# Kernel tuning notes

Measured on AMD Instinct MI355X. Metric: run time of the kernel, lower is better.

The kernel has to match this reference:

```python
import jax, jax.numpy as jnp
import numpy as np

NUM_HEADS = 16
ROPE_THETA = 10000.0


def apply_rope(x):
    # x: (B, H, T, hd), interleaved-pair RoPE (rotary-embedding-torch convention)
    T, hd = x.shape[-2], x.shape[-1]
    inv_freq = 1.0 / (ROPE_THETA ** (jnp.arange(0, hd, 2, dtype=jnp.float32) / hd))  # (hd/2,)
    ang = jnp.arange(T, dtype=jnp.float32)[:, None] * inv_freq[None, :]  # (T, hd/2)
    cos, sin = jnp.cos(ang), jnp.sin(ang)
    x1 = x[..., 0::2]
    x2 = x[..., 1::2]
    r1 = x1 * cos - x2 * sin
    r2 = x1 * sin + x2 * cos
    return jnp.stack([r1, r2], axis=-1).reshape(x.shape)


def setup_inputs() -> dict:
    key = jax.random.key(0)
    ks = jax.random.split(key, 8)
    L, S, B, E = 2048, 2048, 2, 1024
    sc = 1.0 / np.sqrt(E)
    return {
        "query": jax.random.normal(ks[0], (L, B, E), jnp.float32),
        "key": jax.random.normal(ks[1], (S, B, E), jnp.float32),
        "value": jax.random.normal(ks[2], (S, B, E), jnp.float32),
        "key_padding_mask": jnp.zeros((B, S), dtype=bool),
        "Wq": jax.random.normal(ks[3], (E, E), jnp.float32) * sc,
        "bq": jnp.zeros((E,), jnp.float32),
        "Wk": jax.random.normal(ks[4], (E, E), jnp.float32) * sc,
        "bk": jnp.zeros((E,), jnp.float32),
        "Wv": jax.random.normal(ks[5], (E, E), jnp.float32) * sc,
        "bv": jnp.zeros((E,), jnp.float32),
        "Wo": jax.random.normal(ks[6], (E, E), jnp.float32) * sc,
        "bo": jnp.zeros((E,), jnp.float32),
    }


def reference(query, key, value, key_padding_mask, Wq, bq, Wk, bk, Wv, bv, Wo, bo):
    L, B, E = query.shape
    S = key.shape[0]
    H = NUM_HEADS
    hd = E // H
    # projections (torch Linear: x @ W.T + b)
    Q = query @ Wq.T + bq  # (L, B, E)
    K = key @ Wk.T + bk    # (S, B, E)
    V = value @ Wv.T + bv  # (S, B, E)
    # (T, B, E) -> (B, H, T, hd)
    Q = Q.reshape(L, B, H, hd).transpose(1, 2, 0, 3)
    K = K.reshape(S, B, H, hd).transpose(1, 2, 0, 3)
    V = V.reshape(S, B, H, hd).transpose(1, 2, 0, 3)
    Q = apply_rope(Q)
    K = apply_rope(K)
    scores = jnp.einsum("bhld,bhsd->bhls", Q, K) / jnp.sqrt(jnp.float32(hd))
    scores = jnp.where(key_padding_mask[:, None, None, :], -jnp.inf, scores)
    attn = jax.nn.softmax(scores, axis=-1)
    out = jnp.einsum("bhls,bhsd->bhld", attn, V)  # (B, H, L, hd)
    out = out.transpose(2, 0, 1, 3).reshape(L, B, E)
    return out @ Wo.T + bo
```

## Files before the change

kernel.cpp:

```cpp
#include <hip/hip_runtime.h>
#include <hip/hip_bf16.h>

typedef __hip_bfloat16 bf16;
typedef short bf16x8 __attribute__((ext_vector_type(8)));
typedef float f32x4 __attribute__((ext_vector_type(4)));
typedef short s4 __attribute__((ext_vector_type(4)));

#define LL 2048
#define SS 2048
#define EE 1024
#define HH 16
#define HD 64
#define MM (LL * 2)

static __device__ __forceinline__ short f2bs(float f) {
  bf16 h = __float2bfloat16(f);
  short u;
  __builtin_memcpy(&u, &h, 2);
  return u;
}

static __device__ __forceinline__ void st8(bf16* p, float4 x, float4 y) {
  bf16x8 v;
  v[0] = f2bs(x.x); v[1] = f2bs(x.y); v[2] = f2bs(x.z); v[3] = f2bs(x.w);
  v[4] = f2bs(y.x); v[5] = f2bs(y.y); v[6] = f2bs(y.z); v[7] = f2bs(y.w);
  *(bf16x8*)p = v;
}

#define GLL16(gp, lp) __builtin_amdgcn_global_load_lds(                        \
    (const __attribute__((address_space(1))) void*)(gp),                       \
    (__attribute__((address_space(3))) void*)(lp), 16, 0, 0)

__global__ __launch_bounds__(256) void prep_kernel(
    float2* __restrict__ tab, const unsigned char* __restrict__ m,
    float* __restrict__ mf,
    const float* __restrict__ s0, const float* __restrict__ s1,
    const float* __restrict__ s2, const float* __restrict__ s3,
    bf16* __restrict__ wdst) {
  const int bid = blockIdx.x;
  if (bid < 256) {
    int i = bid * 256 + threadIdx.x;
    int pos = i >> 5, fi = i & 31;
    float freq = expf(-(float)fi * (9.210340371976184f / 32.0f));
    float ang = (float)pos * freq;
    float s, c;
    sincosf(ang, &s, &c);
    tab[i] = make_float2(c, s);
  } else if (bid < 272) {
    int i = (bid - 256) * 256 + threadIdx.x;
    if (i < 2 * SS) mf[i] = m[i] ? -1e30f : 0.f;
  } else {
    int b2 = bid - 272;
    int sel = b2 >> 10;
    const float* src = (sel == 0) ? s0 : (sel == 1) ? s1 : (sel == 2) ? s2 : s3;
    size_t loc = ((size_t)(b2 & 1023) * 256 + threadIdx.x) * 4;
    float4 v = *(const float4*)(src + loc);
    s4 p;
    p[0] = f2bs(v.x); p[1] = f2bs(v.y); p[2] = f2bs(v.z); p[3] = f2bs(v.w);
    *(s4*)(wdst + (size_t)sel * EE * EE + loc) = p;
  }
}

template<int MODE, bool XB16, bool WB16>
__global__ __launch_bounds__(256) void proj_kernel(
    const void* __restrict__ Xv, const void* __restrict__ Wv,
    const float* __restrict__ bias, void* __restrict__ dstv,
    const float2* __restrict__ tab)
{
  const int w = threadIdx.x >> 6;
  const int lane = threadIdx.x & 63;
  const int l15 = lane & 15, quad = lane >> 4;
  const int tm = blockIdx.x * 128 + w * 32;
  const int tn = blockIdx.y * 64;

  const size_t aoff0 = (size_t)(tm + l15) * EE + quad * 8;
  const size_t aoff1 = aoff0 + (size_t)16 * EE;
  const size_t woff  = (size_t)(tn + l15) * EE + quad * 8;

  f32x4 zero4 = {0.f, 0.f, 0.f, 0.f};
  f32x4 acc[2][4];
#pragma unroll
  for (int mi = 0; mi < 2; ++mi)
#pragma unroll
    for (int ni = 0; ni < 4; ++ni) acc[mi][ni] = zero4;

  for (int k0 = 0; k0 < EE; k0 += 32) {
    bf16x8 a0, a1;
    if (XB16 || MODE == 3) {
      const bf16* Xb = (const bf16*)Xv;
      a0 = *(const bf16x8*)(Xb + aoff0 + k0);
      a1 = *(const bf16x8*)(Xb + aoff1 + k0);
    } else {
      const float* Xf = (const float*)Xv;
#pragma unroll
      for (int j = 0; j < 8; ++j) a0[j] = f2bs(Xf[aoff0 + k0 + j]);
#pragma unroll
      for (int j = 0; j < 8; ++j) a1[j] = f2bs(Xf[aoff1 + k0 + j]);
    }
#pragma unroll
    for (int ni = 0; ni < 4; ++ni) {
      bf16x8 bv;
      if (WB16) {
        const bf16* Wb = (const bf16*)Wv;
        bv = *(const bf16x8*)(Wb + woff + (size_t)ni * 16 * EE + k0);
      } else {
        const float* Wf = (const float*)Wv;
#pragma unroll
        for (int j = 0; j < 8; ++j) bv[j] = f2bs(Wf[woff + (size_t)ni * 16 * EE + k0 + j]);
      }
      acc[0][ni] = __builtin_amdgcn_mfma_f32_16x16x32_bf16(a0, bv, acc[0][ni], 0, 0, 0);
      acc[1][ni] = __builtin_amdgcn_mfma_f32_16x16x32_bf16(a1, bv, acc[1][ni], 0, 0, 0);
    }
  }

  float bz[4];
#pragma unroll
  for (int ni = 0; ni < 4; ++ni) bz[ni] = bias[tn + ni * 16 + l15];

#pragma unroll
  for (int mi = 0; mi < 2; ++mi) {
#pragma unroll
    for (int ni = 0; ni < 4; ++ni) {
      const int n = tn + ni * 16 + l15;
#pragma unroll
      for (int r = 0; r < 4; ++r) {
        const int m = tm + mi * 16 + quad * 4 + r;
        float v = acc[mi][ni][r] + bz[ni];
        if (MODE <= 1) {
          float other = __shfl_xor(v, 1, 64);
          int pos = m >> 1, b = m & 1, d = n & 63, h = n >> 6;
          float2 cs = tab[pos * 32 + (d >> 1)];
          float rv = (d & 1) ? (other * cs.y + v * cs.x) : (v * cs.x - other * cs.y);
          ((bf16*)dstv)[((size_t)(b * HH + h) * LL + pos) * HD + d] = __float2bfloat16(rv);
        } else if (MODE == 2) {
          int pos = m >> 1, b = m & 1, d = n & 63, h = n >> 6;
          ((bf16*)dstv)[((size_t)(b * HH + h) * HD + d) * SS + pos] = __float2bfloat16(v);
        } else {
          ((float*)dstv)[(size_t)m * EE + n] = v;
        }
      }
    }
  }
}

__global__ __launch_bounds__(256, 6) void qkv_kernel(
    const float* __restrict__ Xq, const float* __restrict__ Xk,
    const float* __restrict__ Xv, const bf16* __restrict__ Wb,
    const float* __restrict__ bq, const float* __restrict__ bk,
    const float* __restrict__ bv, bf16* __restrict__ Qr,
    bf16* __restrict__ Kr, bf16* __restrict__ Vt,
    const float2* __restrict__ tab)
{
  __shared__ __align__(16) bf16 As[2][4096];
  __shared__ __align__(16) bf16 Bs[2][2048];

  const int tid = threadIdx.x;
  const int w = tid >> 6;
  const int lane = tid & 63;
  const int l15 = lane & 15, quad = lane >> 4;
  const int id = blockIdx.x;
  const int z = id >> 9;
  const int g = id & 511;
  const int tmb = (g & 31) * 128;
  const int tn  = (g >> 5) * 64;

  const float* Xf = (z == 0) ? Xq : (z == 1) ? Xk : Xv;
  const bf16* Wm  = Wb + (size_t)z * EE * EE;
  const float* bias = (z == 0) ? bq : (z == 1) ? bk : bv;
  bf16* dst = (z == 0) ? Qr : (z == 1) ? Kr : Vt;

  const int ar = tid >> 2;
  const int akc = tid & 3;
  const float* gA0 = Xf + (size_t)(tmb + ar) * EE + akc * 8;
  const float* gA1 = gA0 + (size_t)64 * EE;
  const int aw0 = (ar >> 1) * 64 + (((((ar & 1) << 2) | akc) ^ ((ar >> 1) & 7)) * 8);
  const int aw1 = aw0 + 2048;

  const int ub = (lane & 7) ^ (lane >> 3);
  const bf16* gB = Wm + (size_t)(tn + w * 16 + 2 * (lane >> 3) + (ub >> 2)) * EE
                      + (ub & 3) * 8;

  const int arbase = (l15 >> 1) * 64 + (((((l15 & 1) << 2) | quad) ^ (l15 >> 1)) * 8);

  f32x4 zero4 = {0.f, 0.f, 0.f, 0.f};
  f32x4 acc[2][4];
#pragma unroll
  for (int mi = 0; mi < 2; ++mi)
#pragma unroll
    for (int ni = 0; ni < 4; ++ni) acc[mi][ni] = zero4;

  {
    float4 a00 = *(const float4*)(gA0);
    float4 a01 = *(const float4*)(gA0 + 4);
    float4 a10 = *(const float4*)(gA1);
    float4 a11 = *(const float4*)(gA1 + 4);
    GLL16(gB, (bf16*)&Bs[0][w * 512] + lane * 8);
    st8(&As[0][aw0], a00, a01);
    st8(&As[0][aw1], a10, a11);
  }
  __syncthreads();

  for (int t = 0; t < 32; ++t) {
    const int cur = t & 1;
    float4 a00, a01, a10, a11;
    if (t < 31) {
      const int k0 = (t + 1) * 32;
      a00 = *(const float4*)(gA0 + k0);
      a01 = *(const float4*)(gA0 + k0 + 4);
      a10 = *(const float4*)(gA1 + k0);
      a11 = *(const float4*)(gA1 + k0 + 4);
      GLL16(gB + k0, (bf16*)&Bs[cur ^ 1][w * 512] + lane * 8);
    }
    bf16x8 af0 = *(const bf16x8*)(&As[cur][w * 1024 + arbase]);
    bf16x8 af1 = *(const bf16x8*)(&As[cur][w * 1024 + 512 + arbase]);
#pragma unroll
    for (int ni = 0; ni < 4; ++ni) {
      bf16x8 bfr = *(const bf16x8*)(&Bs[cur][ni * 512 + arbase]);
      acc[0][ni] = __builtin_amdgcn_mfma_f32_16x16x32_bf16(af0, bfr, acc[0][ni], 0, 0, 0);
      acc[1][ni] = __builtin_amdgcn_mfma_f32_16x16x32_bf16(af1, bfr, acc[1][ni], 0, 0, 0);
    }
    if (t < 31) {
      st8(&As[cur ^ 1][aw0], a00, a01);
      st8(&As[cur ^ 1][aw1], a10, a11);
    }
    __syncthreads();
  }

  float bz[4];
#pragma unroll
  for (int ni = 0; ni < 4; ++ni) bz[ni] = bias[tn + ni * 16 + l15];

#pragma unroll
  for (int mi = 0; mi < 2; ++mi) {
#pragma unroll
    for (int ni = 0; ni < 4; ++ni) {
      const int n = tn + ni * 16 + l15;
#pragma unroll
      for (int r = 0; r < 4; ++r) {
        const int m = tmb + w * 32 + mi * 16 + quad * 4 + r;
        float v = acc[mi][ni][r] + bz[ni];
        if (z <= 1) {
          float other = __shfl_xor(v, 1, 64);
          int pos = m >> 1, b = m & 1, d = n & 63, h = n >> 6;
          float2 cs = tab[pos * 32 + (d >> 1)];
          float rv = (d & 1) ? (other * cs.y + v * cs.x) : (v * cs.x - other * cs.y);
          dst[((size_t)(b * HH + h) * LL + pos) * HD + d] = __float2bfloat16(rv);
        } else {
          int pos = m >> 1, b = m & 1, d = n & 63, h = n >> 6;
          dst[((size_t)(b * HH + h) * HD + d) * SS + pos] = __float2bfloat16(v);
        }
      }
    }
  }
}

__global__ __launch_bounds__(256, 4) void projo_kernel(
    const bf16* __restrict__ X, const bf16* __restrict__ W,
    const float* __restrict__ bias, float* __restrict__ dst)
{
  __shared__ __align__(16) bf16 As[2][64 * 64];
  __shared__ __align__(16) bf16 Bs[2][64 * 64];

  const int tid = threadIdx.x;
  const int w = tid >> 6;
  const int lane = tid & 63;
  const int l15 = lane & 15, quad = lane >> 4;
  const int tmb = blockIdx.x * 64;
  const int tn  = blockIdx.y * 64;

  const int srow = lane >> 3;
  const int gswz = ((lane & 7) ^ srow) * 8;
  const bf16* gA0 = X + (size_t)(tmb + w * 16 + srow) * EE + gswz;
  const bf16* gA1 = gA0 + (size_t)8 * EE;
  const bf16* gB0 = W + (size_t)(tn + w * 16 + srow) * EE + gswz;
  const bf16* gB1 = gB0 + (size_t)8 * EE;

  const int ksw0 = ((quad    ) ^ (l15 & 7)) * 8;
  const int ksw1 = ((quad + 4) ^ (l15 & 7)) * 8;

  f32x4 zero4 = {0.f, 0.f, 0.f, 0.f};
  f32x4 acc[4];
#pragma unroll
  for (int ni = 0; ni < 4; ++ni) acc[ni] = zero4;

  GLL16(gA0, (bf16*)&As[0][(w * 16) * 64] + lane * 8);
  GLL16(gA1, (bf16*)&As[0][(w * 16 + 8) * 64] + lane * 8);
  GLL16(gB0, (bf16*)&Bs[0][(w * 16) * 64] + lane * 8);
  GLL16(gB1, (bf16*)&Bs[0][(w * 16 + 8) * 64] + lane * 8);
  __syncthreads();

  for (int t = 0; t < 16; ++t) {
    const int cur = t & 1;
    if (t < 15) {
      const int k0 = (t + 1) * 64;
      GLL16(gA0 + k0, (bf16*)&As[cur ^ 1][(w * 16) * 64] + lane * 8);
      GLL16(gA1 + k0, (bf16*)&As[cur ^ 1][(w * 16 + 8) * 64] + lane * 8);
      GLL16(gB0 + k0, (bf16*)&Bs[cur ^ 1][(w * 16) * 64] + lane * 8);
      GLL16(gB1 + k0, (bf16*)&Bs[cur ^ 1][(w * 16 + 8) * 64] + lane * 8);
    }
    bf16x8 a0 = *(const bf16x8*)(&As[cur][(w * 16 + l15) * 64 + ksw0]);
    bf16x8 a1 = *(const bf16x8*)(&As[cur][(w * 16 + l15) * 64 + ksw1]);
#pragma unroll
    for (int ni = 0; ni < 4; ++ni) {
      bf16x8 b0 = *(const bf16x8*)(&Bs[cur][(ni * 16 + l15) * 64 + ksw0]);
      bf16x8 b1 = *(const bf16x8*)(&Bs[cur][(ni * 16 + l15) * 64 + ksw1]);
      acc[ni] = __builtin_amdgcn_mfma_f32_16x16x32_bf16(a0, b0, acc[ni], 0, 0, 0);
      acc[ni] = __builtin_amdgcn_mfma_f32_16x16x32_bf16(a1, b1, acc[ni], 0, 0, 0);
    }
    __syncthreads();
  }

  float bz[4];
#pragma unroll
  for (int ni = 0; ni < 4; ++ni) bz[ni] = bias[tn + ni * 16 + l15];

#pragma unroll
  for (int ni = 0; ni < 4; ++ni) {
    const int n = tn + ni * 16 + l15;
#pragma unroll
    for (int r = 0; r < 4; ++r) {
      const int m = tmb + w * 16 + quad * 4 + r;
      dst[(size_t)m * EE + n] = acc[ni][r] + bz[ni];
    }
  }
}

__global__ __launch_bounds__(256, 4) void attn_kernel(
    const bf16* __restrict__ Qr, const bf16* __restrict__ Kr,
    const bf16* __restrict__ Vt, const float* __restrict__ maskf,
    bf16* __restrict__ ctx)
{
  __shared__ __align__(16) bf16 Ks[2][64 * 64];
  __shared__ __align__(16) bf16 Vs[2][64 * 64];
  __shared__ __align__(16) short Plds[4][16][56];

  const int w = threadIdx.x >> 6;
  const int lane = threadIdx.x & 63;
  const int l15 = lane & 15, quad = lane >> 4;
  const int id = blockIdx.x;
  const int bh = id & 31;
  const int qt = id >> 5;
  const int b = bh >> 4, h = bh & 15;
  const int q0 = qt * 64 + w * 16;

  const bf16* Qbh = Qr + (size_t)bh * LL * HD;
  const bf16* Kbh = Kr + (size_t)bh * SS * HD;
  const bf16* Vbh = Vt + (size_t)bh * HD * SS;
  const float* mrow = maskf + b * SS;

  bf16x8 qf0, qf1;
  {
    const bf16* qp = Qbh + (size_t)(q0 + l15) * HD + quad * 8;
    qf0 = *(const bf16x8*)(qp);
    qf1 = *(const bf16x8*)(qp + 32);
  }

  const int srow = lane >> 3;
  const int gswz = ((lane & 7) ^ srow) * 8;
  const int kswz0 = ((quad    ) ^ (l15 & 7)) * 8;
  const int kswz1 = ((quad + 4) ^ (l15 & 7)) * 8;

#define STAGE(buf, S0) {                                                       \
    _Pragma("unroll")                                                          \
    for (int i = 0; i < 2; ++i) {                                              \
      const int rb = w * 16 + i * 8;                                           \
      GLL16(Kbh + (size_t)((S0) + rb + srow) * HD + gswz,                      \
            (bf16*)&Ks[buf][rb * 64] + lane * 8);                              \
      GLL16(Vbh + (size_t)(rb + srow) * SS + (S0) + gswz,                      \
            (bf16*)&Vs[buf][rb * 64] + lane * 8);                              \
    }                                                                          \
  }

  f32x4 zero4 = {0.f, 0.f, 0.f, 0.f};
  f32x4 o[4];
#pragma unroll
  for (int t = 0; t < 4; ++t) o[t] = zero4;
  float ps = 0.f;

  STAGE(0, 0);
  __syncthreads();

  for (int t = 0; t < SS / 64; ++t) {
    const int s0 = t * 64;
    const int cur = t & 1;
    if (t + 1 < SS / 64) STAGE(cur ^ 1, s0 + 64);

#pragma unroll
    for (int ss = 0; ss < 2; ++ss) {
      const bf16* Kb = &Ks[cur][ss * 32 * 64];
      bf16x8 kf00 = *(const bf16x8*)(Kb + (l15)      * 64 + kswz0);
      bf16x8 kf01 = *(const bf16x8*)(Kb + (l15)      * 64 + kswz1);
      bf16x8 kf10 = *(const bf16x8*)(Kb + (16 + l15) * 64 + kswz0);
      bf16x8 kf11 = *(const bf16x8*)(Kb + (16 + l15) * 64 + kswz1);
      bf16x8 vf[4];
#pragma unroll
      for (int tt = 0; tt < 4; ++tt)
        vf[tt] = *(const bf16x8*)(&Vs[cur][0] + (tt * 16 + l15) * 64 +
                                  (((ss * 4 + quad) ^ (l15 & 7)) * 8));
      f32x4 mv0 = *(const f32x4*)(mrow + s0 + ss * 32 + quad * 4);
      f32x4 mv1 = *(const f32x4*)(mrow + s0 + ss * 32 + 16 + quad * 4);

      f32x4 sc0 = zero4, sc1 = zero4;
      sc0 = __builtin_amdgcn_mfma_f32_16x16x32_bf16(kf00, qf0, sc0, 0, 0, 0);
      sc0 = __builtin_amdgcn_mfma_f32_16x16x32_bf16(kf01, qf1, sc0, 0, 0, 0);
      sc1 = __builtin_amdgcn_mfma_f32_16x16x32_bf16(kf10, qf0, sc1, 0, 0, 0);
      sc1 = __builtin_amdgcn_mfma_f32_16x16x32_bf16(kf11, qf1, sc1, 0, 0, 0);
      s4 pk0, pk1;
#pragma unroll
      for (int r = 0; r < 4; ++r) {
        float p = __expf(sc0[r] * 0.125f + mv0[r]);
        ps += p; pk0[r] = f2bs(p);
      }
#pragma unroll
      for (int r = 0; r < 4; ++r) {
        float p = __expf(sc1[r] * 0.125f + mv1[r]);
        ps += p; pk1[r] = f2bs(p);
      }
      *(s4*)&Plds[w][l15][quad * 4] = pk0;
      *(s4*)&Plds[w][l15][16 + quad * 4] = pk1;
      asm volatile("" ::: "memory");
      bf16x8 pf = *(const bf16x8*)&Plds[w][l15][quad * 8];
#pragma unroll
      for (int tt = 0; tt < 4; ++tt)
        o[tt] = __builtin_amdgcn_mfma_f32_16x16x32_bf16(pf, vf[tt], o[tt], 0, 0, 0);
      asm volatile("" ::: "memory");
    }
    __syncthreads();
  }
#undef STAGE

  float lv = ps;
  lv += __shfl_xor(lv, 16, 64);
  lv += __shfl_xor(lv, 32, 64);

#pragma unroll
  for (int r = 0; r < 4; ++r) {
    float li = __shfl(lv, quad * 4 + r, 64);
    float inv = 1.0f / li;
    int q = q0 + quad * 4 + r;
#pragma unroll
    for (int t = 0; t < 4; ++t) {
      float val = o[t][r] * inv;
      ctx[(size_t)(q * 2 + b) * EE + (size_t)h * 64 + t * 16 + l15] = __float2bfloat16(val);
    }
  }
}

extern "C" void kernel_launch(void* const* d_in, const int* in_sizes, int n_in,
                              void* d_out, int out_size, void* d_ws, size_t ws_size,
                              hipStream_t stream) {
  const float* query = (const float*)d_in[0];
  const float* key   = (const float*)d_in[1];
  const float* value = (const float*)d_in[2];
  const unsigned char* mask = (const unsigned char*)d_in[3];
  const float* Wq = (const float*)d_in[4];
  const float* bq = (const float*)d_in[5];
  const float* Wk = (const float*)d_in[6];
  const float* bk = (const float*)d_in[7];
  const float* Wv = (const float*)d_in[8];
  const float* bv = (const float*)d_in[9];
  const float* Wo = (const float*)d_in[10];
  const float* bo = (const float*)d_in[11];

  char* ws = (char*)d_ws;
  const bool big = ws_size >= ((size_t)41 << 20);

  float2* tab   = (float2*)ws;
  float*  maskf = (float*)(ws + (512 << 10));
  bf16* Wb  = (bf16*)(ws + ((size_t)1 << 20));
  size_t base = big ? ((size_t)9 << 20) : ((size_t)1 << 20);
  bf16* Qr  = (bf16*)(ws + base);
  bf16* Kr  = (bf16*)(ws + base + ((size_t)8 << 20));
  bf16* Vt  = (bf16*)(ws + base + ((size_t)16 << 20));
  bf16* ctx = (bf16*)(ws + base + ((size_t)24 << 20));

  prep_kernel<<<big ? 4368 : 272, 256, 0, stream>>>(
      tab, mask, maskf, Wq, Wk, Wv, Wo, Wb);

  if (big) {
    qkv_kernel<<<1536, 256, 0, stream>>>(query, key, value, Wb, bq, bk, bv,
                                         Qr, Kr, Vt, tab);
  } else {
    dim3 gp(MM / 128, EE / 64);
    proj_kernel<0, false, false><<<gp, 256, 0, stream>>>(query, Wq, bq, Qr, tab);
    proj_kernel<1, false, false><<<gp, 256, 0, stream>>>(key,   Wk, bk, Kr, tab);
    proj_kernel<2, false, false><<<gp, 256, 0, stream>>>(value, Wv, bv, Vt, tab);
  }

  attn_kernel<<<(LL / 64) * 2 * HH, 256, 0, stream>>>(Qr, Kr, Vt, maskf, ctx);

  if (big) {
    dim3 go(MM / 64, EE / 64);
    projo_kernel<<<go, 256, 0, stream>>>(ctx, Wb + (size_t)3 * EE * EE, bo, (float*)d_out);
  } else {
    dim3 gp(MM / 128, EE / 64);
    proj_kernel<3, true, false><<<gp, 256, 0, stream>>>(ctx, Wo, bo, d_out, tab);
  }
}
```

Baseline: 249.2 us.

## Drop prep kernel: convert weights in-GEMM, compute RoPE inline, read byte mask directly

Removes the separate prep kernel that precomputed a RoPE sin/cos table, a float mask and bf16 weight copies. The QKV and output projection kernels now load fp32 weights and convert them to bf16 while staging into LDS. RoPE angles are computed with sincosf in the epilogue, and the attention kernel expands the byte mask on the fly. This saves one launch and a pass over the weights, but replaces async global-to-LDS copies with register-staged fp32 loads, which doubles weight bytes read per tile and adds transcendental work in the epilogue.

```diff
diff --git a/kernel.cpp b/kernel.cpp
--- a/kernel.cpp
+++ b/kernel.cpp
@@ -31,125 +31,14 @@
     (const __attribute__((address_space(1))) void*)(gp),                       \
     (__attribute__((address_space(3))) void*)(lp), 16, 0, 0)
 
-__global__ __launch_bounds__(256) void prep_kernel(
-    float2* __restrict__ tab, const unsigned char* __restrict__ m,
-    float* __restrict__ mf,
-    const float* __restrict__ s0, const float* __restrict__ s1,
-    const float* __restrict__ s2, const float* __restrict__ s3,
-    bf16* __restrict__ wdst) {
-  const int bid = blockIdx.x;
-  if (bid < 256) {
-    int i = bid * 256 + threadIdx.x;
-    int pos = i >> 5, fi = i & 31;
-    float freq = expf(-(float)fi * (9.210340371976184f / 32.0f));
-    float ang = (float)pos * freq;
-    float s, c;
-    sincosf(ang, &s, &c);
-    tab[i] = make_float2(c, s);
-  } else if (bid < 272) {
-    int i = (bid - 256) * 256 + threadIdx.x;
-    if (i < 2 * SS) mf[i] = m[i] ? -1e30f : 0.f;
-  } else {
-    int b2 = bid - 272;
-    int sel = b2 >> 10;
-    const float* src = (sel == 0) ? s0 : (sel == 1) ? s1 : (sel == 2) ? s2 : s3;
-    size_t loc = ((size_t)(b2 & 1023) * 256 + threadIdx.x) * 4;
-    float4 v = *(const float4*)(src + loc);
-    s4 p;
-    p[0] = f2bs(v.x); p[1] = f2bs(v.y); p[2] = f2bs(v.z); p[3] = f2bs(v.w);
-    *(s4*)(wdst + (size_t)sel * EE * EE + loc) = p;
-  }
-}
-
-template<int MODE, bool XB16, bool WB16>
-__global__ __launch_bounds__(256) void proj_kernel(
-    const void* __restrict__ Xv, const void* __restrict__ Wv,
-    const float* __restrict__ bias, void* __restrict__ dstv,
-    const float2* __restrict__ tab)
-{
-  const int w = threadIdx.x >> 6;
-  const int lane = threadIdx.x & 63;
-  const int l15 = lane & 15, quad = lane >> 4;
-  const int tm = blockIdx.x * 128 + w * 32;
-  const int tn = blockIdx.y * 64;
-
-  const size_t aoff0 = (size_t)(tm + l15) * EE + quad * 8;
-  const size_t aoff1 = aoff0 + (size_t)16 * EE;
-  const size_t woff  = (size_t)(tn + l15) * EE + quad * 8;
-
-  f32x4 zero4 = {0.f, 0.f, 0.f, 0.f};
-  f32x4 acc[2][4];
-#pragma unroll
-  for (int mi = 0; mi < 2; ++mi)
-#pragma unroll
-    for (int ni = 0; ni < 4; ++ni) acc[mi][ni] = zero4;
-
-  for (int k0 = 0; k0 < EE; k0 += 32) {
-    bf16x8 a0, a1;
-    if (XB16 || MODE == 3) {
-      const bf16* Xb = (const bf16*)Xv;
-      a0 = *(const bf16x8*)(Xb + aoff0 + k0);
-      a1 = *(const bf16x8*)(Xb + aoff1 + k0);
-    } else {
-      const float* Xf = (const float*)Xv;
-#pragma unroll
-      for (int j = 0; j < 8; ++j) a0[j] = f2bs(Xf[aoff0 + k0 + j]);
-#pragma unroll
-      for (int j = 0; j < 8; ++j) a1[j] = f2bs(Xf[aoff1 + k0 + j]);
-    }
-#pragma unroll
-    for (int ni = 0; ni < 4; ++ni) {
-      bf16x8 bv;
-      if (WB16) {
-        const bf16* Wb = (const bf16*)Wv;
-        bv = *(const bf16x8*)(Wb + woff + (size_t)ni * 16 * EE + k0);
-      } else {
-        const float* Wf = (const float*)Wv;
-#pragma unroll
-        for (int j = 0; j < 8; ++j) bv[j] = f2bs(Wf[woff + (size_t)ni * 16 * EE + k0 + j]);
-      }
-      acc[0][ni] = __builtin_amdgcn_mfma_f32_16x16x32_bf16(a0, bv, acc[0][ni], 0, 0, 0);
-      acc[1][ni] = __builtin_amdgcn_mfma_f32_16x16x32_bf16(a1, bv, acc[1][ni], 0, 0, 0);
-    }
-  }
-
-  float bz[4];
-#pragma unroll
-  for (int ni = 0; ni < 4; ++ni) bz[ni] = bias[tn + ni * 16 + l15];
-
-#pragma unroll
-  for (int mi = 0; mi < 2; ++mi) {
-#pragma unroll
-    for (int ni = 0; ni < 4; ++ni) {
-      const int n = tn + ni * 16 + l15;
-#pragma unroll
-      for (int r = 0; r < 4; ++r) {
-        const int m = tm + mi * 16 + quad * 4 + r;
-        float v = acc[mi][ni][r] + bz[ni];
-        if (MODE <= 1) {
-          float other = __shfl_xor(v, 1, 64);
-          int pos = m >> 1, b = m & 1, d = n & 63, h = n >> 6;
-          float2 cs = tab[pos * 32 + (d >> 1)];
-          float rv = (d & 1) ? (other * cs.y + v * cs.x) : (v * cs.x - other * cs.y);
-          ((bf16*)dstv)[((size_t)(b * HH + h) * LL + pos) * HD + d] = __float2bfloat16(rv);
-        } else if (MODE == 2) {
-          int pos = m >> 1, b = m & 1, d = n & 63, h = n >> 6;
-          ((bf16*)dstv)[((size_t)(b * HH + h) * HD + d) * SS + pos] = __float2bfloat16(v);
-        } else {
-          ((float*)dstv)[(size_t)m * EE + n] = v;
-        }
-      }
-    }
-  }
-}
-
 __global__ __launch_bounds__(256, 6) void qkv_kernel(
     const float* __restrict__ Xq, const float* __restrict__ Xk,
-    const float* __restrict__ Xv, const bf16* __restrict__ Wb,
+    const float* __restrict__ Xv,
+    const float* __restrict__ Wq, const float* __restrict__ Wk,
+    const float* __restrict__ Wv,
     const float* __restrict__ bq, const float* __restrict__ bk,
     const float* __restrict__ bv, bf16* __restrict__ Qr,
-    bf16* __restrict__ Kr, bf16* __restrict__ Vt,
-    const float2* __restrict__ tab)
+    bf16* __restrict__ Kr, bf16* __restrict__ Vt)
 {
   __shared__ __align__(16) bf16 As[2][4096];
   __shared__ __align__(16) bf16 Bs[2][2048];
@@ -165,7 +54,7 @@
   const int tn  = (g >> 5) * 64;
 
   const float* Xf = (z == 0) ? Xq : (z == 1) ? Xk : Xv;
-  const bf16* Wm  = Wb + (size_t)z * EE * EE;
+  const float* Wf = (z == 0) ? Wq : (z == 1) ? Wk : Wv;
   const float* bias = (z == 0) ? bq : (z == 1) ? bk : bv;
   bf16* dst = (z == 0) ? Qr : (z == 1) ? Kr : Vt;
 
@@ -176,9 +65,8 @@
   const int aw0 = (ar >> 1) * 64 + (((((ar & 1) << 2) | akc) ^ ((ar >> 1) & 7)) * 8);
   const int aw1 = aw0 + 2048;
 
-  const int ub = (lane & 7) ^ (lane >> 3);
-  const bf16* gB = Wm + (size_t)(tn + w * 16 + 2 * (lane >> 3) + (ub >> 2)) * EE
-                      + (ub & 3) * 8;
+  const float* gB = Wf + (size_t)(tn + ar) * EE + akc * 8;
+  const int bw0 = aw0;
 
   const int arbase = (l15 >> 1) * 64 + (((((l15 & 1) << 2) | quad) ^ (l15 >> 1)) * 8);
 
@@ -194,22 +82,25 @@
     float4 a01 = *(const float4*)(gA0 + 4);
     float4 a10 = *(const float4*)(gA1);
     float4 a11 = *(const float4*)(gA1 + 4);
-    GLL16(gB, (bf16*)&Bs[0][w * 512] + lane * 8);
+    float4 b00 = *(const float4*)(gB);
+    float4 b01 = *(const float4*)(gB + 4);
     st8(&As[0][aw0], a00, a01);
     st8(&As[0][aw1], a10, a11);
+    st8(&Bs[0][bw0], b00, b01);
   }
   __syncthreads();
 
   for (int t = 0; t < 32; ++t) {
     const int cur = t & 1;
-    float4 a00, a01, a10, a11;
+    float4 a00, a01, a10, a11, b00, b01;
     if (t < 31) {
       const int k0 = (t + 1) * 32;
       a00 = *(const float4*)(gA0 + k0);
       a01 = *(const float4*)(gA0 + k0 + 4);
       a10 = *(const float4*)(gA1 + k0);
       a11 = *(const float4*)(gA1 + k0 + 4);
-      GLL16(gB + k0, (bf16*)&Bs[cur ^ 1][w * 512] + lane * 8);
+      b00 = *(const float4*)(gB + k0);
+      b01 = *(const float4*)(gB + k0 + 4);
     }
     bf16x8 af0 = *(const bf16x8*)(&As[cur][w * 1024 + arbase]);
     bf16x8 af1 = *(const bf16x8*)(&As[cur][w * 1024 + 512 + arbase]);
@@ -222,6 +113,7 @@
     if (t < 31) {
       st8(&As[cur ^ 1][aw0], a00, a01);
       st8(&As[cur ^ 1][aw1], a10, a11);
+      st8(&Bs[cur ^ 1][bw0], b00, b01);
     }
     __syncthreads();
   }
@@ -230,22 +122,45 @@
 #pragma unroll
   for (int ni = 0; ni < 4; ++ni) bz[ni] = bias[tn + ni * 16 + l15];
 
-#pragma unroll
-  for (int mi = 0; mi < 2; ++mi) {
+  if (z <= 1) {
+    const int B0h = (tmb + w * 32 + quad * 4) >> 1;
 #pragma unroll
     for (int ni = 0; ni < 4; ++ni) {
       const int n = tn + ni * 16 + l15;
-#pragma unroll
-      for (int r = 0; r < 4; ++r) {
-        const int m = tmb + w * 32 + mi * 16 + quad * 4 + r;
-        float v = acc[mi][ni][r] + bz[ni];
-        if (z <= 1) {
+      const int fi = (ni * 16 + l15) >> 1;
+      float freq = expf(-(float)fi * (9.210340371976184f / 32.0f));
+      float cc[4], sn[4];
+#pragma unroll
+      for (int pp = 0; pp < 4; ++pp) {
+        int pos = B0h + (pp >> 1) * 8 + (pp & 1);
+        sincosf((float)pos * freq, &sn[pp], &cc[pp]);
+      }
+#pragma unroll
+      for (int mi = 0; mi < 2; ++mi) {
+#pragma unroll
+        for (int r = 0; r < 4; ++r) {
+          const int m = tmb + w * 32 + mi * 16 + quad * 4 + r;
+          float v = acc[mi][ni][r] + bz[ni];
           float other = __shfl_xor(v, 1, 64);
+          const int pi = mi * 2 + (r >> 1);
           int pos = m >> 1, b = m & 1, d = n & 63, h = n >> 6;
-          float2 cs = tab[pos * 32 + (d >> 1)];
-          float rv = (d & 1) ? (other * cs.y + v * cs.x) : (v * cs.x - other * cs.y);
-          dst[((size_t)(b * HH + h) * LL + pos) * HD + d] = __float2bfloat16(rv);
-        } else {
+          (void)pos;
+          float rv = (d & 1) ? (other * sn[pi] + v * cc[pi])
+                             : (v * cc[pi] - other * sn[pi]);
+          dst[((size_t)(b * HH + h) * LL + (m >> 1)) * HD + d] = __float2bfloat16(rv);
+        }
+      }
+    }
+  } else {
+#pragma unroll
+    for (int mi = 0; mi < 2; ++mi) {
+#pragma unroll
+      for (int ni = 0; ni < 4; ++ni) {
+        const int n = tn + ni * 16 + l15;
+#pragma unroll
+        for (int r = 0; r < 4; ++r) {
+          const int m = tmb + w * 32 + mi * 16 + quad * 4 + r;
+          float v = acc[mi][ni][r] + bz[ni];
           int pos = m >> 1, b = m & 1, d = n & 63, h = n >> 6;
           dst[((size_t)(b * HH + h) * HD + d) * SS + pos] = __float2bfloat16(v);
         }
@@ -255,7 +170,7 @@
 }
 
 __global__ __launch_bounds__(256, 4) void projo_kernel(
-    const bf16* __restrict__ X, const bf16* __restrict__ W,
+    const bf16* __restrict__ X, const float* __restrict__ W,
     const float* __restrict__ bias, float* __restrict__ dst)
 {
   __shared__ __align__(16) bf16 As[2][64 * 64];
@@ -272,8 +187,13 @@
   const int gswz = ((lane & 7) ^ srow) * 8;
   const bf16* gA0 = X + (size_t)(tmb + w * 16 + srow) * EE + gswz;
   const bf16* gA1 = gA0 + (size_t)8 * EE;
-  const bf16* gB0 = W + (size_t)(tn + w * 16 + srow) * EE + gswz;
-  const bf16* gB1 = gB0 + (size_t)8 * EE;
+
+  const int wr = tid >> 2;
+  const int wc = tid & 3;
+  const float* gW0 = W + (size_t)(tn + wr) * EE + wc * 8;
+  const float* gW1 = gW0 + 32;
+  const int bw0 = wr * 64 + ((wc       ^ (wr & 7)) * 8);
+  const int bw1 = wr * 64 + (((wc | 4) ^ (wr & 7)) * 8);
 
   const int ksw0 = ((quad    ) ^ (l15 & 7)) * 8;
   const int ksw1 = ((quad + 4) ^ (l15 & 7)) * 8;
@@ -283,20 +203,29 @@
 #pragma unroll
   for (int ni = 0; ni < 4; ++ni) acc[ni] = zero4;
 
-  GLL16(gA0, (bf16*)&As[0][(w * 16) * 64] + lane * 8);
-  GLL16(gA1, (bf16*)&As[0][(w * 16 + 8) * 64] + lane * 8);
-  GLL16(gB0, (bf16*)&Bs[0][(w * 16) * 64] + lane * 8);
-  GLL16(gB1, (bf16*)&Bs[0][(w * 16 + 8) * 64] + lane * 8);
+  {
+    GLL16(gA0, (bf16*)&As[0][(w * 16) * 64] + lane * 8);
+    GLL16(gA1, (bf16*)&As[0][(w * 16 + 8) * 64] + lane * 8);
+    float4 w00 = *(const float4*)(gW0);
+    float4 w01 = *(const float4*)(gW0 + 4);
+    float4 w10 = *(const float4*)(gW1);
+    float4 w11 = *(const float4*)(gW1 + 4);
+    st8(&Bs[0][bw0], w00, w01);
+    st8(&Bs[0][bw1], w10, w11);
+  }
   __syncthreads();
 
   for (int t = 0; t < 16; ++t) {
     const int cur = t & 1;
+    float4 w00, w01, w10, w11;
     if (t < 15) {
       const int k0 = (t + 1) * 64;
       GLL16(gA0 + k0, (bf16*)&As[cur ^ 1][(w * 16) * 64] + lane * 8);
       GLL16(gA1 + k0, (bf16*)&As[cur ^ 1][(w * 16 + 8) * 64] + lane * 8);
-      GLL16(gB0 + k0, (bf16*)&Bs[cur ^ 1][(w * 16) * 64] + lane * 8);
-      GLL16(gB1 + k0, (bf16*)&Bs[cur ^ 1][(w * 16 + 8) * 64] + lane * 8);
+      w00 = *(const float4*)(gW0 + k0);
+      w01 = *(const float4*)(gW0 + k0 + 4);
+      w10 = *(const float4*)(gW1 + k0);
+      w11 = *(const float4*)(gW1 + k0 + 4);
     }
     bf16x8 a0 = *(const bf16x8*)(&As[cur][(w * 16 + l15) * 64 + ksw0]);
     bf16x8 a1 = *(const bf16x8*)(&As[cur][(w * 16 + l15) * 64 + ksw1]);
@@ -307,6 +236,10 @@
       acc[ni] = __builtin_amdgcn_mfma_f32_16x16x32_bf16(a0, b0, acc[ni], 0, 0, 0);
       acc[ni] = __builtin_amdgcn_mfma_f32_16x16x32_bf16(a1, b1, acc[ni], 0, 0, 0);
     }
+    if (t < 15) {
+      st8(&Bs[cur ^ 1][bw0], w00, w01);
+      st8(&Bs[cur ^ 1][bw1], w10, w11);
+    }
     __syncthreads();
   }
 
@@ -327,7 +260,7 @@
 
 __global__ __launch_bounds__(256, 4) void attn_kernel(
     const bf16* __restrict__ Qr, const bf16* __restrict__ Kr,
-    const bf16* __restrict__ Vt, const float* __restrict__ maskf,
+    const bf16* __restrict__ Vt, const unsigned char* __restrict__ maskb,
     bf16* __restrict__ ctx)
 {
   __shared__ __align__(16) bf16 Ks[2][64 * 64];
@@ -346,7 +279,7 @@
   const bf16* Qbh = Qr + (size_t)bh * LL * HD;
   const bf16* Kbh = Kr + (size_t)bh * SS * HD;
   const bf16* Vbh = Vt + (size_t)bh * HD * SS;
-  const float* mrow = maskf + b * SS;
+  const unsigned char* mrow = maskb + b * SS;
 
   bf16x8 qf0, qf1;
   {
@@ -397,8 +330,13 @@
       for (int tt = 0; tt < 4; ++tt)
         vf[tt] = *(const bf16x8*)(&Vs[cur][0] + (tt * 16 + l15) * 64 +
                                   (((ss * 4 + quad) ^ (l15 & 7)) * 8));
-      f32x4 mv0 = *(const f32x4*)(mrow + s0 + ss * 32 + quad * 4);
-      f32x4 mv1 = *(const f32x4*)(mrow + s0 + ss * 32 + 16 + quad * 4);
+      uchar4 u0 = *(const uchar4*)(mrow + s0 + ss * 32 + quad * 4);
+      uchar4 u1 = *(const uchar4*)(mrow + s0 + ss * 32 + 16 + quad * 4);
+      f32x4 mv0, mv1;
+      mv0[0] = u0.x ? -1e30f : 0.f; mv0[1] = u0.y ? -1e30f : 0.f;
+      mv0[2] = u0.z ? -1e30f : 0.f; mv0[3] = u0.w ? -1e30f : 0.f;
+      mv1[0] = u1.x ? -1e30f : 0.f; mv1[1] = u1.y ? -1e30f : 0.f;
+      mv1[2] = u1.z ? -1e30f : 0.f; mv1[3] = u1.w ? -1e30f : 0.f;
 
       f32x4 sc0 = zero4, sc1 = zero4;
       sc0 = __builtin_amdgcn_mfma_f32_16x16x32_bf16(kf00, qf0, sc0, 0, 0, 0);
@@ -463,37 +401,18 @@
   const float* bo = (const float*)d_in[11];
 
   char* ws = (char*)d_ws;
-  const bool big = ws_size >= ((size_t)41 << 20);
-
-  float2* tab   = (float2*)ws;
-  float*  maskf = (float*)(ws + (512 << 10));
-  bf16* Wb  = (bf16*)(ws + ((size_t)1 << 20));
-  size_t base = big ? ((size_t)9 << 20) : ((size_t)1 << 20);
-  bf16* Qr  = (bf16*)(ws + base);
-  bf16* Kr  = (bf16*)(ws + base + ((size_t)8 << 20));
-  bf16* Vt  = (bf16*)(ws + base + ((size_t)16 << 20));
-  bf16* ctx = (bf16*)(ws + base + ((size_t)24 << 20));
-
-  prep_kernel<<<big ? 4368 : 272, 256, 0, stream>>>(
-      tab, mask, maskf, Wq, Wk, Wv, Wo, Wb);
-
-  if (big) {
-    qkv_kernel<<<1536, 256, 0, stream>>>(query, key, value, Wb, bq, bk, bv,
-                                         Qr, Kr, Vt, tab);
-  } else {
-    dim3 gp(MM / 128, EE / 64);
-    proj_kernel<0, false, false><<<gp, 256, 0, stream>>>(query, Wq, bq, Qr, tab);
-    proj_kernel<1, false, false><<<gp, 256, 0, stream>>>(key,   Wk, bk, Kr, tab);
-    proj_kernel<2, false, false><<<gp, 256, 0, stream>>>(value, Wv, bv, Vt, tab);
-  }
-
-  attn_kernel<<<(LL / 64) * 2 * HH, 256, 0, stream>>>(Qr, Kr, Vt, maskf, ctx);
-
-  if (big) {
-    dim3 go(MM / 64, EE / 64);
-    projo_kernel<<<go, 256, 0, stream>>>(ctx, Wb + (size_t)3 * EE * EE, bo, (float*)d_out);
-  } else {
-    dim3 gp(MM / 128, EE / 64);
-    proj_kernel<3, true, false><<<gp, 256, 0, stream>>>(ctx, Wo, bo, d_out, tab);
-  }
-}
+  (void)ws_size; (void)in_sizes; (void)n_in; (void)out_size;
+
+  bf16* Qr  = (bf16*)ws;
+  bf16* Kr  = (bf16*)(ws + ((size_t)8 << 20));
+  bf16* Vt  = (bf16*)(ws + ((size_t)16 << 20));
+  bf16* ctx = (bf16*)(ws + ((size_t)24 << 20));
+
+  qkv_kernel<<<1536, 256, 0, stream>>>(query, key, value, Wq, Wk, Wv,
+                                       bq, bk, bv, Qr, Kr, Vt);
+
+  attn_kernel<<<(LL / 64) * 2 * HH, 256, 0, stream>>>(Qr, Kr, Vt, mask, ctx);
+
+  dim3 go(MM / 64, EE / 64);
+  projo_kernel<<<go, 256, 0, stream>>>(ctx, Wo, bo, (float*)d_out);
+}
```

Result: slower. 280.6 us (+12.6%).
